# Performance work log

Hardware: AMD Instinct MI355X
Metric: run time of the kernel (lower is better)

## Reference

```python
import jax, jax.numpy as jnp
import numpy as np

B, S, E = 4, 2048, 1024
H = 16
D = E // H  # head_dim = 64


def setup_inputs() -> dict:
    key = jax.random.key(0)
    ks = jax.random.split(key, 7)
    query = jax.random.normal(ks[0], (B, S, E), dtype=jnp.float32)
    k_in = jax.random.normal(ks[1], (B, S, E), dtype=jnp.float32)
    v_in = jax.random.normal(ks[2], (B, S, E), dtype=jnp.float32)
    lim_qkv = 1.0 / np.sqrt(E)
    W_qkv = jax.random.uniform(ks[3], (E, 3 * E), jnp.float32, -lim_qkv, lim_qkv)
    b_qkv = jax.random.uniform(ks[4], (3 * E,), jnp.float32, -lim_qkv, lim_qkv)
    W_out = jax.random.uniform(ks[5], (E, E), jnp.float32, -lim_qkv, lim_qkv)
    b_out = jax.random.uniform(ks[6], (E,), jnp.float32, -lim_qkv, lim_qkv)
    return {"query": query, "key": k_in, "value": v_in,
            "W_qkv": W_qkv, "b_qkv": b_qkv, "W_out": W_out, "b_out": b_out}


def reference(query, key, value, W_qkv, b_qkv, W_out, b_out):
    # NOTE: original module ignores key/value; q,k,v all derived from query.
    b, s, e = query.shape
    qkv = query @ W_qkv + b_qkv                     # [B,S,3E]
    qkv = qkv.reshape(b, s, 3, H, D)
    q, k, v = qkv[:, :, 0], qkv[:, :, 1], qkv[:, :, 2]   # [B,S,H,D]
    scale = jnp.sqrt(jnp.asarray(D, dtype=jnp.float32))
    scores = jnp.einsum('bqhd,bkhd->bhqk', q, k) / scale  # [B,H,S,S]
    attn = jax.nn.softmax(scores, axis=-1)
    out = jnp.einsum('bhqk,bkhd->bqhd', attn, v).reshape(b, s, e)
    return out @ W_out + b_out
```

## Files before the change

### kernel.cpp

```cpp
#include <hip/hip_runtime.h>
#include <hip/hip_bf16.h>

#define Bc 4
#define Sc 2048
#define Ec 1024
#define Hc 16
#define Dc 64

typedef __bf16 bf16_t;
typedef __bf16 bf16x4 __attribute__((ext_vector_type(4)));
typedef __bf16 bf16x8 __attribute__((ext_vector_type(8)));
typedef float f32x4 __attribute__((ext_vector_type(4)));

extern "C" __device__ float __ocml_native_exp2_f32(float);

__device__ __forceinline__ f32x4 mfma16(bf16x8 a, bf16x8 b, f32x4 c) {
    return __builtin_amdgcn_mfma_f32_16x16x32_bf16(a, b, c, 0, 0, 0);
}

__device__ __forceinline__ void gload16(const bf16_t* g, bf16_t* l) {
    __builtin_amdgcn_global_load_lds(
        (const __attribute__((address_space(1))) unsigned int*)g,
        (__attribute__((address_space(3))) unsigned int*)l, 16, 0, 0);
}

__global__ __launch_bounds__(256)
void cvt_bf16(const float* __restrict__ in, bf16_t* __restrict__ out, int n4)
{
    int i = blockIdx.x * 256 + threadIdx.x;
    if (i >= n4) return;
    float4 v = ((const float4*)in)[i];
    alignas(8) bf16_t o[4];
    o[0] = (bf16_t)v.x; o[1] = (bf16_t)v.y; o[2] = (bf16_t)v.z; o[3] = (bf16_t)v.w;
    ((uint2*)out)[i] = *(uint2*)o;
}

__global__ __launch_bounds__(256)
void transpose_w(const float* __restrict__ W, bf16_t* __restrict__ Wt, int K, int N)
{
    __shared__ float T[64][65];
    const int kt = blockIdx.y, nt = blockIdx.x;
    const int r = threadIdx.x >> 4;
    const int c = (threadIdx.x & 15) * 4;
    #pragma unroll
    for (int p = 0; p < 4; p++) {
        float4 v = *(const float4*)(W + (size_t)(kt*64 + r + p*16)*N + nt*64 + c);
        T[r + p*16][c] = v.x; T[r + p*16][c+1] = v.y;
        T[r + p*16][c+2] = v.z; T[r + p*16][c+3] = v.w;
    }
    __syncthreads();
    #pragma unroll
    for (int p = 0; p < 4; p++) {
        int n = nt*64 + r + p*16;
        alignas(8) bf16_t tmp[4];
        #pragma unroll
        for (int j = 0; j < 4; j++) tmp[j] = (bf16_t)T[c + j][r + p*16];
        *(uint2*)(Wt + (size_t)n*K + kt*64 + c) = *(uint2*)tmp;
    }
}

__global__ __launch_bounds__(256)
void transpose_v(const bf16_t* __restrict__ qkv, bf16_t* __restrict__ vt)
{
    __shared__ bf16_t T[64][72];
    const int bh = blockIdx.y, st = blockIdx.x;
    const int b = bh >> 4, h = bh & 15;
    const int sr = threadIdx.x >> 3;
    const int dc = (threadIdx.x & 7) * 8;
    #pragma unroll
    for (int p = 0; p < 2; p++) {
        const bf16_t* src = qkv + (size_t)(b*Sc + st*64 + sr + p*32)*(3*Ec) + 2*Ec + h*Dc + dc;
        *(uint4*)&T[sr + p*32][dc] = *(const uint4*)src;
    }
    __syncthreads();
    const int dr = threadIdx.x >> 3;
    const int sc2 = (threadIdx.x & 7) * 8;
    #pragma unroll
    for (int p = 0; p < 2; p++) {
        alignas(16) bf16_t tmp[8];
        #pragma unroll
        for (int j = 0; j < 8; j++)
            tmp[j] = T[sc2 + j][dr + p*32];
        *(uint4*)(vt + (size_t)bh*Dc*Sc + (size_t)(dr + p*32)*Sc + st*64 + sc2) = *(uint4*)tmp;
    }
}

template<int OUT_IS_F32>
__global__ __launch_bounds__(256)
void gemm_bt(const bf16_t* __restrict__ A, const bf16_t* __restrict__ Bt,
             const float* __restrict__ biasp, void* __restrict__ Cp,
             int M, int N, int K)
{
    __shared__ bf16_t As[2][128*32];
    __shared__ bf16_t Bs[2][128*32];

    const int tid  = threadIdx.x;
    const int wave = tid >> 6;
    const int lane = tid & 63;
    const int quad = lane >> 4;
    const int l16  = lane & 15;
    const int wm   = (wave >> 1) * 64;
    const int wn   = (wave & 1) * 64;
    const int m0   = blockIdx.y * 128;
    const int n0   = blockIdx.x * 128;

    const int srow = wave*32 + (lane >> 2);
    const int scol = (lane & 3) * 8;
    const bf16_t* ap0 = A  + (size_t)(m0 + srow)      * K + scol;
    const bf16_t* ap1 = A  + (size_t)(m0 + srow + 16) * K + scol;
    const bf16_t* bp0 = Bt + (size_t)(n0 + srow)      * K + scol;
    const bf16_t* bp1 = Bt + (size_t)(n0 + srow + 16) * K + scol;
    bf16_t* asl0 = &As[0][(wave*32)      * 32];
    bf16_t* asl1 = &As[0][(wave*32 + 16) * 32];
    bf16_t* bsl0 = &Bs[0][(wave*32)      * 32];
    bf16_t* bsl1 = &Bs[0][(wave*32 + 16) * 32];
    bf16_t* asl2 = &As[1][(wave*32)      * 32];
    bf16_t* asl3 = &As[1][(wave*32 + 16) * 32];
    bf16_t* bsl2 = &Bs[1][(wave*32)      * 32];
    bf16_t* bsl3 = &Bs[1][(wave*32 + 16) * 32];

    f32x4 acc[4][4] = {};

    for (int k0 = 0; k0 < K; k0 += 64) {
        gload16(ap0 + k0,      asl0);
        gload16(ap1 + k0,      asl1);
        gload16(ap0 + k0 + 32, asl2);
        gload16(ap1 + k0 + 32, asl3);
        gload16(bp0 + k0,      bsl0);
        gload16(bp1 + k0,      bsl1);
        gload16(bp0 + k0 + 32, bsl2);
        gload16(bp1 + k0 + 32, bsl3);
        __syncthreads();

        #pragma unroll
        for (int kc = 0; kc < 2; kc++) {
            bf16x8 af[4], bfr[4];
            #pragma unroll
            for (int mi = 0; mi < 4; mi++)
                af[mi] = *(const bf16x8*)&As[kc][(wm + mi*16 + l16)*32 + quad*8];
            #pragma unroll
            for (int ni = 0; ni < 4; ni++)
                bfr[ni] = *(const bf16x8*)&Bs[kc][(wn + ni*16 + l16)*32 + quad*8];
            #pragma unroll
            for (int mi = 0; mi < 4; mi++)
                #pragma unroll
                for (int ni = 0; ni < 4; ni++)
                    acc[mi][ni] = mfma16(af[mi], bfr[ni], acc[mi][ni]);
        }
        __syncthreads();
    }

    float bv[4];
    #pragma unroll
    for (int ni = 0; ni < 4; ni++) bv[ni] = biasp[n0 + wn + ni*16 + l16];

    #pragma unroll
    for (int mi = 0; mi < 4; mi++)
        #pragma unroll
        for (int ni = 0; ni < 4; ni++)
            #pragma unroll
            for (int r = 0; r < 4; r++) {
                int row = m0 + wm + mi*16 + quad*4 + r;
                int col = n0 + wn + ni*16 + l16;
                float v = acc[mi][ni][r] + bv[ni];
                if (OUT_IS_F32) ((float*)Cp)[(size_t)row * N + col] = v;
                else            ((bf16_t*)Cp)[(size_t)row * N + col] = (bf16_t)v;
            }
}

__global__ __launch_bounds__(256, 2)
void attn8(const bf16_t* __restrict__ qkv, const bf16_t* __restrict__ vt,
           bf16_t* __restrict__ aout)
{
    __shared__ bf16_t Ks[64][72];
    __shared__ bf16_t Vs[64][72];
    __shared__ bf16_t Po[4][16][72];

    const int tid  = threadIdx.x;
    const int wave = tid >> 6;
    const int lane = tid & 63;
    const int quad = lane >> 4;
    const int l16  = lane & 15;
    const int bh   = blockIdx.y;
    const int b    = bh >> 4;
    const int h    = bh & 15;
    const int qt   = blockIdx.x;
    const float kscale = 0.125f * 1.44269504088896340736f;

    bf16x8 qf[4][2];
    #pragma unroll
    for (int qi = 0; qi < 4; qi++) {
        const bf16_t* qrow = qkv + (size_t)(b*Sc + qt*256 + wave*64 + qi*16 + l16)*(3*Ec) + h*Dc;
        qf[qi][0] = *(const bf16x8*)(qrow + quad*8);
        qf[qi][1] = *(const bf16x8*)(qrow + 32 + quad*8);
        #pragma unroll
        for (int f = 0; f < 2; f++)
            #pragma unroll
            for (int e = 0; e < 8; e++)
                qf[qi][f][e] = (bf16_t)((float)qf[qi][f][e] * kscale);
    }

    f32x4 acc[4][4] = {};
    float lpart[4] = {};

    const int krw   = tid >> 2;
    const int dbase = (tid & 3) * 16;

    const bf16_t* kbase = qkv + (size_t)(b*Sc + krw)*(3*Ec) + Ec + h*Dc + dbase;
    const bf16_t* vbase = vt + (size_t)bh*Dc*Sc + (size_t)krw*Sc + dbase;
    const size_t kstep = (size_t)64 * (3*Ec);
    uint4 ku0 = ((const uint4*)kbase)[0];
    uint4 ku1 = ((const uint4*)kbase)[1];
    uint4 vu0 = ((const uint4*)vbase)[0];
    uint4 vu1 = ((const uint4*)vbase)[1];

    for (int kt = 0; kt < Sc/64; kt++) {
        __syncthreads();
        *(uint4*)&Ks[krw][dbase]     = ku0;
        *(uint4*)&Ks[krw][dbase + 8] = ku1;
        *(uint4*)&Vs[krw][dbase]     = vu0;
        *(uint4*)&Vs[krw][dbase + 8] = vu1;
        __syncthreads();

        if (kt < Sc/64 - 1) {
            const bf16_t* kn = kbase + (size_t)(kt+1) * kstep;
            const bf16_t* vn = vbase + (kt+1) * 64;
            ku0 = ((const uint4*)kn)[0];
            ku1 = ((const uint4*)kn)[1];
            vu0 = ((const uint4*)vn)[0];
            vu1 = ((const uint4*)vn)[1];
        }

        bf16x8 kf[4][2];
        #pragma unroll
        for (int ki = 0; ki < 4; ki++) {
            kf[ki][0] = *(const bf16x8*)&Ks[ki*16 + l16][quad*8];
            kf[ki][1] = *(const bf16x8*)&Ks[ki*16 + l16][32 + quad*8];
        }

        bf16x4 pp[4][4];
        #pragma unroll
        for (int ki = 0; ki < 4; ki++) {
            #pragma unroll
            for (int qi = 0; qi < 4; qi++) {
                f32x4 z = {};
                z = mfma16(kf[ki][0], qf[qi][0], z);
                z = mfma16(kf[ki][1], qf[qi][1], z);
                float p0 = __ocml_native_exp2_f32(z[0]);
                float p1 = __ocml_native_exp2_f32(z[1]);
                float p2 = __ocml_native_exp2_f32(z[2]);
                float p3 = __ocml_native_exp2_f32(z[3]);
                lpart[qi] += (p0 + p1) + (p2 + p3);
                bf16x4 w;
                w[0] = (bf16_t)p0; w[1] = (bf16_t)p1;
                w[2] = (bf16_t)p2; w[3] = (bf16_t)p3;
                pp[ki][qi] = w;
            }
        }

        #pragma unroll
        for (int c = 0; c < 2; c++) {
            bf16x8 pcat[4];
            #pragma unroll
            for (int qi = 0; qi < 4; qi++)
                pcat[qi] = __builtin_shufflevector(pp[2*c][qi], pp[2*c+1][qi],
                                                   0,1,2,3,4,5,6,7);
            #pragma unroll
            for (int di = 0; di < 4; di++) {
                bf16x4 v0 = *(const bf16x4*)&Vs[di*16 + l16][c*32 + 4*quad];
                bf16x4 v1 = *(const bf16x4*)&Vs[di*16 + l16][c*32 + 16 + 4*quad];
                bf16x8 vf = __builtin_shufflevector(v0, v1, 0,1,2,3,4,5,6,7);
                #pragma unroll
                for (int qi = 0; qi < 4; qi++)
                    acc[di][qi] = mfma16(vf, pcat[qi], acc[di][qi]);
            }
        }
    }

    float inv[4];
    #pragma unroll
    for (int qi = 0; qi < 4; qi++) {
        float l = lpart[qi];
        l += __shfl_xor(l, 16);
        l += __shfl_xor(l, 32);
        inv[qi] = 1.0f / l;
    }

    const int qrd  = lane >> 2;
    const int dch  = (lane & 3) * 16;
    #pragma unroll
    for (int qi = 0; qi < 4; qi++) {
        #pragma unroll
        for (int di = 0; di < 4; di++) {
            alignas(8) bf16_t w[4];
            #pragma unroll
            for (int r = 0; r < 4; r++)
                w[r] = (bf16_t)(acc[di][qi][r] * inv[qi]);
            *(uint2*)&Po[wave][l16][di*16 + quad*4] = *(uint2*)w;
        }
        asm volatile("s_waitcnt lgkmcnt(0)" ::: "memory");
        uint4 o0 = *(const uint4*)&Po[wave][qrd][dch];
        uint4 o1 = *(const uint4*)&Po[wave][qrd][dch + 8];
        bf16_t* dst = aout + (size_t)(b*Sc + qt*256 + wave*64 + qi*16 + qrd)*Ec + h*Dc + dch;
        ((uint4*)dst)[0] = o0;
        ((uint4*)dst)[1] = o1;
    }
}

extern "C" void kernel_launch(void* const* d_in, const int* in_sizes, int n_in,
                              void* d_out, int out_size, void* d_ws, size_t ws_size,
                              hipStream_t stream) {
    const float* query = (const float*)d_in[0];
    const float* W_qkv = (const float*)d_in[3];
    const float* b_qkv = (const float*)d_in[4];
    const float* W_out = (const float*)d_in[5];
    const float* b_out = (const float*)d_in[6];
    float* out = (float*)d_out;

    const size_t MT = (size_t)Bc * Sc;
    char* ws = (char*)d_ws;
    size_t off = 0;
    bf16_t* qbf    = (bf16_t*)(ws + off); off += MT*Ec*2;
    bf16_t* qkv_ws = (bf16_t*)(ws + off); off += MT*3*Ec*2;
    bf16_t* vt_ws  = (bf16_t*)(ws + off); off += MT*Ec*2;
    bf16_t* wqkv_t = (bf16_t*)(ws + off); off += (size_t)3*Ec*Ec*2;
    bf16_t* wout_t = (bf16_t*)(ws + off); off += (size_t)Ec*Ec*2;

    cvt_bf16<<<(MT*Ec/4 + 255)/256, 256, 0, stream>>>(query, qbf, (int)(MT*Ec/4));
    transpose_w<<<dim3(3*Ec/64, Ec/64), 256, 0, stream>>>(W_qkv, wqkv_t, Ec, 3*Ec);
    transpose_w<<<dim3(Ec/64, Ec/64), 256, 0, stream>>>(W_out, wout_t, Ec, Ec);

    gemm_bt<0><<<dim3(3*Ec/128, MT/128), 256, 0, stream>>>(
        qbf, wqkv_t, b_qkv, qkv_ws, (int)MT, 3*Ec, Ec);

    transpose_v<<<dim3(Sc/64, Bc*Hc), 256, 0, stream>>>(qkv_ws, vt_ws);

    attn8<<<dim3(Sc/256, Bc*Hc), 256, 0, stream>>>(qkv_ws, vt_ws, qbf);

    gemm_bt<1><<<dim3(Ec/128, MT/128), 256, 0, stream>>>(
        qbf, wout_t, b_out, out, (int)MT, Ec, Ec);
}
```

Measured before the change: 305.6 us.

## Replace QKV projection GEMM with 256-wide, 512-thread pipelined kernel

Adds a new gemm256 kernel for the QKV projection. It uses a 128x256 output tile, 8 waves, K-tiles of 64, and double-buffered direct global-to-LDS loads. An interleaved schedule splits each K-step into four quarter MFMA phases, with staged prefetch, barriers and setprio, so loads overlap compute and each LDS byte is reused more. This adds LDS pressure (96KB) and a fragile hand-tuned synchronisation scheme, and it may lower occupancy.

```diff
diff --git a/kernel.cpp b/kernel.cpp
--- a/kernel.cpp
+++ b/kernel.cpp
@@ -23,6 +23,9 @@
         (const __attribute__((address_space(1))) unsigned int*)g,
         (__attribute__((address_space(3))) unsigned int*)l, 16, 0, 0);
 }
+
+#define FENCE asm volatile("" ::: "memory")
+#define BARRIER do { FENCE; __builtin_amdgcn_s_barrier(); FENCE; } while (0)
 
 __global__ __launch_bounds__(256)
 void cvt_bf16(const float* __restrict__ in, bf16_t* __restrict__ out, int n4)
@@ -83,6 +86,145 @@
             tmp[j] = T[sc2 + j][dr + p*32];
         *(uint4*)(vt + (size_t)bh*Dc*Sc + (size_t)(dr + p*32)*Sc + st*64 + sc2) = *(uint4*)tmp;
     }
+}
+
+__global__ __launch_bounds__(512)
+void gemm256(const bf16_t* __restrict__ A, const bf16_t* __restrict__ Bt,
+             const float* __restrict__ biasp, bf16_t* __restrict__ C,
+             int M, int N, int K)
+{
+    __shared__ bf16_t LA[2][128*64];
+    __shared__ bf16_t LB[2][256*64];
+
+    const int tid  = threadIdx.x;
+    const int wave = tid >> 6;
+    const int lane = tid & 63;
+    const int quad = lane >> 4;
+    const int l16  = lane & 15;
+    const int wm   = (wave >> 2) * 64;
+    const int wn   = (wave & 3) * 64;
+    const int m0   = blockIdx.y * 128;
+    const int n0   = blockIdx.x * 256;
+
+    const int qsw   = (quad ^ ((l16 >> 1) & 2)) * 8;
+    const int sch   = ((lane & 7) ^ ((lane >> 4) & 2)) * 8;
+    const int srow8 = wave*8 + (lane >> 3);
+
+    const int NT = K >> 6;
+
+    f32x4 acc[4][4] = {};
+    bf16x8 a0[2][2], a1[2][2], b0[2][2], b1[2][2];
+
+    auto stageA = [&](int buf, int kt, int crow) {
+        gload16(A + (size_t)(m0 + crow + srow8)*K + kt*64 + sch,
+                &LA[buf][(crow + wave*8)*64]);
+    };
+    auto stageB = [&](int buf, int kt, int crow) {
+        gload16(Bt + (size_t)(n0 + crow + srow8)*K + kt*64 + sch,
+                &LB[buf][(crow + wave*8)*64]);
+    };
+
+    stageB(0, 0, 0);   stageB(0, 0, 64);
+    stageB(0, 0, 128); stageB(0, 0, 192);
+    stageA(0, 0, 0);   stageA(0, 0, 64);
+    stageB(1, 1, 0);   stageB(1, 1, 64);
+    stageA(1, 1, 0);   stageA(1, 1, 64);
+    asm volatile("s_waitcnt vmcnt(4)" ::: "memory");
+    BARRIER;
+
+    for (int g = 0; g < NT; ++g) {
+        const int buf = g & 1;
+        #pragma unroll
+        for (int mi = 0; mi < 2; mi++)
+            #pragma unroll
+            for (int kk = 0; kk < 2; kk++)
+                a0[mi][kk] = *(const bf16x8*)&LA[buf][(wm + mi*16 + l16)*64 + kk*32 + qsw];
+        #pragma unroll
+        for (int ni = 0; ni < 2; ni++)
+            #pragma unroll
+            for (int kk = 0; kk < 2; kk++)
+                b0[ni][kk] = *(const bf16x8*)&LB[buf][(wn + ni*16 + l16)*64 + kk*32 + qsw];
+        if (g + 1 < NT) { stageB(buf^1, g+1, 128); stageB(buf^1, g+1, 192); }
+        BARRIER;
+        asm volatile("s_waitcnt lgkmcnt(0)" ::: "memory");
+        __builtin_amdgcn_sched_barrier(0);
+        __builtin_amdgcn_s_setprio(1);
+        #pragma unroll
+        for (int mi = 0; mi < 2; mi++)
+            #pragma unroll
+            for (int ni = 0; ni < 2; ni++)
+                #pragma unroll
+                for (int kk = 0; kk < 2; kk++)
+                    acc[mi][ni] = mfma16(a0[mi][kk], b0[ni][kk], acc[mi][ni]);
+        __builtin_amdgcn_s_setprio(0);
+        BARRIER;
+        #pragma unroll
+        for (int ni = 0; ni < 2; ni++)
+            #pragma unroll
+            for (int kk = 0; kk < 2; kk++)
+                b1[ni][kk] = *(const bf16x8*)&LB[buf][(wn + 32 + ni*16 + l16)*64 + kk*32 + qsw];
+        BARRIER;
+        asm volatile("s_waitcnt lgkmcnt(0)" ::: "memory");
+        __builtin_amdgcn_sched_barrier(0);
+        __builtin_amdgcn_s_setprio(1);
+        #pragma unroll
+        for (int mi = 0; mi < 2; mi++)
+            #pragma unroll
+            for (int ni = 0; ni < 2; ni++)
+                #pragma unroll
+                for (int kk = 0; kk < 2; kk++)
+                    acc[mi][2+ni] = mfma16(a0[mi][kk], b1[ni][kk], acc[mi][2+ni]);
+        __builtin_amdgcn_s_setprio(0);
+        BARRIER;
+        #pragma unroll
+        for (int mi = 0; mi < 2; mi++)
+            #pragma unroll
+            for (int kk = 0; kk < 2; kk++)
+                a1[mi][kk] = *(const bf16x8*)&LA[buf][(wm + 32 + mi*16 + l16)*64 + kk*32 + qsw];
+        if (g + 2 < NT) { stageB(buf, g+2, 0); stageB(buf, g+2, 64); }
+        BARRIER;
+        asm volatile("s_waitcnt lgkmcnt(0)" ::: "memory");
+        __builtin_amdgcn_sched_barrier(0);
+        __builtin_amdgcn_s_setprio(1);
+        #pragma unroll
+        for (int mi = 0; mi < 2; mi++)
+            #pragma unroll
+            for (int ni = 0; ni < 2; ni++)
+                #pragma unroll
+                for (int kk = 0; kk < 2; kk++)
+                    acc[2+mi][2+ni] = mfma16(a1[mi][kk], b1[ni][kk], acc[2+mi][2+ni]);
+        __builtin_amdgcn_s_setprio(0);
+        BARRIER;
+        if (g + 2 < NT) { stageA(buf, g+2, 0); stageA(buf, g+2, 64); }
+        BARRIER;
+        __builtin_amdgcn_s_setprio(1);
+        #pragma unroll
+        for (int mi = 0; mi < 2; mi++)
+            #pragma unroll
+            for (int ni = 0; ni < 2; ni++)
+                #pragma unroll
+                for (int kk = 0; kk < 2; kk++)
+                    acc[2+mi][ni] = mfma16(a1[mi][kk], b0[ni][kk], acc[2+mi][ni]);
+        __builtin_amdgcn_s_setprio(0);
+        asm volatile("s_waitcnt vmcnt(4)" ::: "memory");
+        BARRIER;
+    }
+
+    float bv[4];
+    #pragma unroll
+    for (int ni = 0; ni < 4; ni++)
+        bv[ni] = biasp[n0 + wn + (ni>>1)*32 + (ni&1)*16 + l16];
+
+    #pragma unroll
+    for (int mi = 0; mi < 4; mi++)
+        #pragma unroll
+        for (int ni = 0; ni < 4; ni++)
+            #pragma unroll
+            for (int r = 0; r < 4; r++) {
+                int row = m0 + wm + (mi>>1)*32 + (mi&1)*16 + quad*4 + r;
+                int col = n0 + wn + (ni>>1)*32 + (ni&1)*16 + l16;
+                C[(size_t)row * N + col] = (bf16_t)(acc[mi][ni][r] + bv[ni]);
+            }
 }
 
 template<int OUT_IS_F32>
@@ -330,7 +472,7 @@
     transpose_w<<<dim3(3*Ec/64, Ec/64), 256, 0, stream>>>(W_qkv, wqkv_t, Ec, 3*Ec);
     transpose_w<<<dim3(Ec/64, Ec/64), 256, 0, stream>>>(W_out, wout_t, Ec, Ec);
 
-    gemm_bt<0><<<dim3(3*Ec/128, MT/128), 256, 0, stream>>>(
+    gemm256<<<dim3(3*Ec/256, MT/128), 512, 0, stream>>>(
         qbf, wqkv_t, b_qkv, qkv_ws, (int)MT, 3*Ec, Ec);
 
     transpose_v<<<dim3(Sc/64, Bc*Hc), 256, 0, stream>>>(qkv_ws, vt_ws);
```

After: 318.8 us. 4.3% more time.

## Rewrite projection GEMMs with triple-buffered LDS pipeline and larger 128x256 tiles

Applied to the files above, without the earlier changes.

Replaces the double-buffered 128x128 GEMM with a 512-thread kernel that computes 128x256 tiles, using a three-stage LDS ring with prefetch two tiles ahead and explicit vmcnt waits and barriers. It also adds an XOR swizzle on LDS columns to reduce bank conflicts, an XCD-aware block remap, and raised wave priority around the MFMA block. The aim is to hide global load latency and cut LDS conflicts in both projection GEMMs. It uses more LDS per block (144KB), which may reduce occupancy, and the hand-tuned waitcnt logic is fragile.

```diff
diff --git a/kernel.cpp b/kernel.cpp
--- a/kernel.cpp
+++ b/kernel.cpp
@@ -23,6 +23,9 @@
         (const __attribute__((address_space(1))) unsigned int*)g,
         (__attribute__((address_space(3))) unsigned int*)l, 16, 0, 0);
 }
+
+#define FENCE asm volatile("" ::: "memory")
+#define BARRIER do { FENCE; __builtin_amdgcn_s_barrier(); FENCE; } while (0)
 
 __global__ __launch_bounds__(256)
 void cvt_bf16(const float* __restrict__ in, bf16_t* __restrict__ out, int n4)
@@ -86,68 +89,92 @@
 }
 
 template<int OUT_IS_F32>
-__global__ __launch_bounds__(256)
-void gemm_bt(const bf16_t* __restrict__ A, const bf16_t* __restrict__ Bt,
-             const float* __restrict__ biasp, void* __restrict__ Cp,
-             int M, int N, int K)
-{
-    __shared__ bf16_t As[2][128*32];
-    __shared__ bf16_t Bs[2][128*32];
+__global__ __launch_bounds__(512)
+void gemm3b(const bf16_t* __restrict__ A, const bf16_t* __restrict__ Bt,
+            const float* __restrict__ biasp, void* __restrict__ Cp,
+            int M, int N, int K)
+{
+    __shared__ bf16_t LS[3][384*64];
 
     const int tid  = threadIdx.x;
     const int wave = tid >> 6;
     const int lane = tid & 63;
     const int quad = lane >> 4;
     const int l16  = lane & 15;
-    const int wm   = (wave >> 1) * 64;
-    const int wn   = (wave & 1) * 64;
-    const int m0   = blockIdx.y * 128;
-    const int n0   = blockIdx.x * 128;
-
-    const int srow = wave*32 + (lane >> 2);
-    const int scol = (lane & 3) * 8;
-    const bf16_t* ap0 = A  + (size_t)(m0 + srow)      * K + scol;
-    const bf16_t* ap1 = A  + (size_t)(m0 + srow + 16) * K + scol;
-    const bf16_t* bp0 = Bt + (size_t)(n0 + srow)      * K + scol;
-    const bf16_t* bp1 = Bt + (size_t)(n0 + srow + 16) * K + scol;
-    bf16_t* asl0 = &As[0][(wave*32)      * 32];
-    bf16_t* asl1 = &As[0][(wave*32 + 16) * 32];
-    bf16_t* bsl0 = &Bs[0][(wave*32)      * 32];
-    bf16_t* bsl1 = &Bs[0][(wave*32 + 16) * 32];
-    bf16_t* asl2 = &As[1][(wave*32)      * 32];
-    bf16_t* asl3 = &As[1][(wave*32 + 16) * 32];
-    bf16_t* bsl2 = &Bs[1][(wave*32)      * 32];
-    bf16_t* bsl3 = &Bs[1][(wave*32 + 16) * 32];
+    const int wm   = (wave >> 2) * 64;
+    const int wn   = (wave & 3) * 64;
+
+    const int nwg = gridDim.x * gridDim.y;
+    const int bid = blockIdx.y * gridDim.x + blockIdx.x;
+    const int cpx = nwg >> 3;
+    const int swz = (bid & 7) * cpx + (bid >> 3);
+    const int nbx = N >> 8;
+    const int m0  = (swz / nbx) * 128;
+    const int n0  = (swz % nbx) * 256;
+
+    const int NT = K >> 6;
+
+    const int srow = lane >> 3;
+    const int sch  = (lane & 7) ^ ((wave*4 + (lane >> 4)) & 7);
+    const bf16_t* aSrc = A  + (size_t)(m0 + wave*8 + srow)*K + sch*8;
+    const bf16_t* bSrc = Bt + (size_t)(n0 + wave*8 + srow)*K + sch*8;
+
+    const int fsw = (l16 >> 1) & 7;
 
     f32x4 acc[4][4] = {};
 
-    for (int k0 = 0; k0 < K; k0 += 64) {
-        gload16(ap0 + k0,      asl0);
-        gload16(ap1 + k0,      asl1);
-        gload16(ap0 + k0 + 32, asl2);
-        gload16(ap1 + k0 + 32, asl3);
-        gload16(bp0 + k0,      bsl0);
-        gload16(bp1 + k0,      bsl1);
-        gload16(bp0 + k0 + 32, bsl2);
-        gload16(bp1 + k0 + 32, bsl3);
-        __syncthreads();
-
-        #pragma unroll
-        for (int kc = 0; kc < 2; kc++) {
-            bf16x8 af[4], bfr[4];
-            #pragma unroll
-            for (int mi = 0; mi < 4; mi++)
-                af[mi] = *(const bf16x8*)&As[kc][(wm + mi*16 + l16)*32 + quad*8];
+    auto stage = [&](int bi, int t) {
+        const bf16_t* ap = aSrc + t*64;
+        const bf16_t* bp = bSrc + t*64;
+        gload16(ap,               &LS[bi][(0         + wave*8)*64]);
+        gload16(ap + (size_t)64*K, &LS[bi][(64        + wave*8)*64]);
+        gload16(bp,               &LS[bi][(128 +   0 + wave*8)*64]);
+        gload16(bp + (size_t)64*K, &LS[bi][(128 +  64 + wave*8)*64]);
+        gload16(bp + (size_t)128*K,&LS[bi][(128 + 128 + wave*8)*64]);
+        gload16(bp + (size_t)192*K,&LS[bi][(128 + 192 + wave*8)*64]);
+    };
+
+    stage(0, 0);
+    stage(1, 1);
+    asm volatile("s_waitcnt vmcnt(6)" ::: "memory");
+    BARRIER;
+
+    int bi = 0;
+    for (int t = 0; t < NT; ++t) {
+        bf16x8 af[4][2], bfr[4][2];
+        #pragma unroll
+        for (int mi = 0; mi < 4; mi++)
+            #pragma unroll
+            for (int kk = 0; kk < 2; kk++)
+                af[mi][kk] = *(const bf16x8*)
+                    &LS[bi][(wm + mi*16 + l16)*64 + ((kk*4+quad)^fsw)*8];
+        #pragma unroll
+        for (int ni = 0; ni < 4; ni++)
+            #pragma unroll
+            for (int kk = 0; kk < 2; kk++)
+                bfr[ni][kk] = *(const bf16x8*)
+                    &LS[bi][(128 + wn + ni*16 + l16)*64 + ((kk*4+quad)^fsw)*8];
+
+        if (t + 2 < NT) {
+            int b2 = bi + 2; if (b2 >= 3) b2 -= 3;
+            stage(b2, t + 2);
+        }
+        BARRIER;
+        asm volatile("s_waitcnt lgkmcnt(0)" ::: "memory");
+        __builtin_amdgcn_sched_barrier(0);
+        __builtin_amdgcn_s_setprio(1);
+        #pragma unroll
+        for (int mi = 0; mi < 4; mi++)
             #pragma unroll
             for (int ni = 0; ni < 4; ni++)
-                bfr[ni] = *(const bf16x8*)&Bs[kc][(wn + ni*16 + l16)*32 + quad*8];
-            #pragma unroll
-            for (int mi = 0; mi < 4; mi++)
                 #pragma unroll
-                for (int ni = 0; ni < 4; ni++)
-                    acc[mi][ni] = mfma16(af[mi], bfr[ni], acc[mi][ni]);
-        }
-        __syncthreads();
+                for (int kk = 0; kk < 2; kk++)
+                    acc[mi][ni] = mfma16(af[mi][kk], bfr[ni][kk], acc[mi][ni]);
+        __builtin_amdgcn_s_setprio(0);
+        if (t + 2 < NT)      asm volatile("s_waitcnt vmcnt(6)" ::: "memory");
+        else if (t + 1 < NT) asm volatile("s_waitcnt vmcnt(0)" ::: "memory");
+        BARRIER;
+        bi = bi + 1; if (bi >= 3) bi = 0;
     }
 
     float bv[4];
@@ -330,13 +357,13 @@
     transpose_w<<<dim3(3*Ec/64, Ec/64), 256, 0, stream>>>(W_qkv, wqkv_t, Ec, 3*Ec);
     transpose_w<<<dim3(Ec/64, Ec/64), 256, 0, stream>>>(W_out, wout_t, Ec, Ec);
 
-    gemm_bt<0><<<dim3(3*Ec/128, MT/128), 256, 0, stream>>>(
+    gemm3b<0><<<dim3(3*Ec/256, MT/128), 512, 0, stream>>>(
         qbf, wqkv_t, b_qkv, qkv_ws, (int)MT, 3*Ec, Ec);
 
     transpose_v<<<dim3(Sc/64, Bc*Hc), 256, 0, stream>>>(qkv_ws, vt_ws);
 
     attn8<<<dim3(Sc/256, Bc*Hc), 256, 0, stream>>>(qkv_ws, vt_ws, qbf);
 
-    gemm_bt<1><<<dim3(Ec/128, MT/128), 256, 0, stream>>>(
+    gemm3b<1><<<dim3(Ec/256, MT/128), 512, 0, stream>>>(
         qbf, wout_t, b_out, out, (int)MT, Ec, Ec);
 }
```

After: 302.0 us. No clear change (-1.2%).
